# Performance work log

Measured on AMD Instinct MI355X. Metric: run time of the kernel, lower is better.

The kernel has to match this reference:

```python
import jax, jax.numpy as jnp
import numpy as np

STEP_PRI = 0.01
STEP_DUAL = 0.01
REG_SP = 0.002
NUM_ITERS = 50
B, N = 512, 64


def _matrix_power(m, p):
    # exponentiation by squaring; p is a static Python int >= 1
    result = jnp.broadcast_to(jnp.eye(m.shape[-1], dtype=m.dtype), m.shape)
    while p > 0:
        if p & 1:
            result = result @ m
        p >>= 1
        if p:
            m = m @ m
    return result


def _matrix_poly(m, d, p):
    # (I + m/d)^p, matching torch matrix_poly
    x = jnp.eye(d, dtype=m.dtype) + m / d
    return _matrix_power(x, p)


def _threshold(x):
    # nn.Threshold(0.5, 0): x if x > 0.5 else 0
    return jnp.where(x > 0.5, x, jnp.zeros_like(x))


def setup_inputs() -> dict:
    key = jax.random.key(0)
    adj = jax.random.uniform(key, (B, N, N), dtype=jnp.float32)
    return {"adj": adj}


def reference(adj):
    n = adj.shape[-1]
    x0 = adj
    scores = _threshold(adj)
    alpha0 = jnp.zeros(adj.shape[0], dtype=adj.dtype)

    def step(carry, _):
        x, alpha = carry
        # grad of augmented Lagrangian (DAG constraint gradient uses (I + x*x/n)^(n-1)^T)
        poly_t = jnp.swapaxes(_matrix_poly(x * x, n, n - 1), -1, -2)
        grad = -scores + 2.0 * alpha[:, None, None] * x * poly_t / n
        til_x = x - STEP_PRI * grad
        # soft-threshold (prox of L1), then clamp to <= 1
        new_x = jax.nn.relu(jnp.abs(til_x) - REG_SP * STEP_PRI)
        x = 1.0 - jax.nn.relu(1.0 - new_x)
        # constraint2: tr((I + x*x/n)^min(30,n)) / n - 1, per batch element
        h = jnp.trace(_matrix_poly(x * x, n, min(30, n)), axis1=-2, axis2=-1) / n - 1.0
        alpha = alpha + STEP_DUAL * h
        return (x, alpha), None

    (x, _), _ = jax.lax.scan(step, (x0, alpha0), None, length=NUM_ITERS)
    return _threshold(x)
```

## Files before the change

kernel.cpp:

```cpp
#include <hip/hip_runtime.h>
#include <stdint.h>

#define PL 4096

typedef unsigned int u32;
typedef unsigned short u16;
typedef float f32x4 __attribute__((ext_vector_type(4)));
typedef short short8 __attribute__((ext_vector_type(8)));
typedef unsigned int u32x2 __attribute__((ext_vector_type(2)));

__device__ __forceinline__ u32 prm(u32 a, u32 b, u32 s) {
  return __builtin_amdgcn_perm(a, b, s);
}
__device__ __forceinline__ u32 pk(float f0, float f1) {
  return prm(__float_as_uint(f1), __float_as_uint(f0), 0x07060302u);
}
__device__ __forceinline__ float rlo(u32 w) { return __uint_as_float(w << 16); }
__device__ __forceinline__ float rhi(u32 w) {
  return __uint_as_float(w & 0xffff0000u);
}
__device__ __forceinline__ short8 mk8(u32 w0, u32 w1, u32 w2, u32 w3) {
  union {
    u32 w[4];
    short8 s;
  } u;
  u.w[0] = w0;
  u.w[1] = w1;
  u.w[2] = w2;
  u.w[3] = w3;
  return u.s;
}
__device__ __forceinline__ void dot8(short8 a, short8 b, float& part) {
  union {
    short8 s;
    u32 w[4];
  } ua, ub;
  ua.s = a;
  ub.s = b;
#pragma unroll
  for (int w = 0; w < 4; ++w) {
    part = fmaf(rlo(ua.w[w]), rlo(ub.w[w]), part);
    part = fmaf(rhi(ua.w[w]), rhi(ub.w[w]), part);
  }
}
__device__ __forceinline__ f32x4 MF(short8 a, short8 b, f32x4 c) {
  return __builtin_amdgcn_mfma_f32_16x16x32_bf16(a, b, c, 0, 0, 0);
}

struct AF {
  short8 a0, a1;
};
struct BF8 {
  short8 b[4][2];
};

__device__ __forceinline__ void dist2(u32 U, u32 V, u32& x, u32& y) {
  u32x2 s = __builtin_amdgcn_permlane32_swap(U, V, false, false);
#if __has_builtin(__builtin_amdgcn_permlane16_swap)
  u32x2 t = __builtin_amdgcn_permlane16_swap(s[0], s[1], false, false);
  x = t[0];
  y = t[1];
#else
  u32 a = s[0], b = s[1];
  u32 bx = (u32)__shfl_xor((int)b, 16);
  u32 ax = (u32)__shfl_xor((int)a, 16);
  const bool odd = ((threadIdx.x >> 4) & 1) != 0;
  x = odd ? bx : a;
  y = odd ? b : ax;
#endif
}

__device__ __forceinline__ AF macc_to_af(const f32x4 (&m)[4]) {
  u32 P0[4], P1[4];
#pragma unroll
  for (int b = 0; b < 4; ++b) {
    P0[b] = pk(m[b][0], m[b][1]);
    P1[b] = pk(m[b][2], m[b][3]);
  }
  u32 W0[4], W1[4];
  dist2(P0[0], P0[1], W0[0], W0[2]);
  dist2(P1[0], P1[1], W0[1], W0[3]);
  dist2(P0[2], P0[3], W1[0], W1[2]);
  dist2(P1[2], P1[3], W1[1], W1[3]);
  AF r;
  r.a0 = mk8(W0[0], W0[1], W0[2], W0[3]);
  r.a1 = mk8(W1[0], W1[1], W1[2], W1[3]);
  return r;
}

__global__ __launch_bounds__(256, 2) void dag_iter_kernel(
    const float* __restrict__ adj, float* __restrict__ out) {
  __shared__ __align__(16) u16 BUF[4 * PL];
  __shared__ float red[4];
  u16* S0 = BUF;
  u16* S1 = BUF + PL;
  u16* S2 = BUF + 2 * PL;
  u16* S3 = BUF + 3 * PL;

  if ((blockIdx.x >> 8) & 1) __builtin_amdgcn_s_sleep(11);

  const int tid = (int)threadIdx.x;
  const int lane = tid & 63;
  const int wv = tid >> 6;
  const int l15 = lane & 15;
  const int grp = lane >> 4;
  const int l7 = l15 & 7;
  const int r0 = (tid & 15) << 2;
  const int c0 = (((tid >> 4) + (tid & 15)) & 15) << 2;

  int ra[2];
#pragma unroll
  for (int kh = 0; kh < 2; ++kh)
    ra[kh] = (16 * wv + l15) * 64 + ((((kh << 2) + grp) ^ l7) << 3);
  int rb[4][2];
#pragma unroll
  for (int b = 0; b < 4; ++b)
#pragma unroll
    for (int kh = 0; kh < 2; ++kh)
      rb[b][kh] = (16 * b + l15) * 64 + ((((kh << 2) + grp) ^ l7) << 3);
  int sT[4];
#pragma unroll
  for (int b = 0; b < 4; ++b)
    sT[b] = (16 * b + l15) * 64 + (((2 * wv + (grp >> 1)) ^ l7) << 3) +
            ((grp & 1) << 2);
  int prow[4], pcol[4];
#pragma unroll
  for (int i = 0; i < 4; ++i) {
    prow[i] = (r0 + i) * 64 + ((((c0 >> 3) ^ ((r0 + i) & 7))) << 3) + (c0 & 7);
    pcol[i] = (c0 + i) * 64 + ((((r0 >> 3) ^ ((c0 + i) & 7))) << 3) + (r0 & 7);
  }

  const float* src = adj + (size_t)blockIdx.x * 4096;
  float x[4][4], sc[4][4];
#pragma unroll
  for (int i = 0; i < 4; ++i) {
    f32x4 v = *(const f32x4*)(src + (r0 + i) * 64 + c0);
#pragma unroll
    for (int j = 0; j < 4; ++j) {
      x[i][j] = v[j];
      sc[i][j] = (v[j] > 0.5f) ? v[j] : 0.0f;
    }
  }
  float alpha = 0.0f;
  AF af;
  BF8 bf3;

  auto loadBF = [&](const u16* P) {
    BF8 f;
#pragma unroll
    for (int b = 0; b < 4; ++b) {
      f.b[b][0] = *(const short8*)(P + rb[b][0]);
      f.b[b][1] = *(const short8*)(P + rb[b][1]);
    }
    return f;
  };
  auto mirrorAF = [&](const AF& a, const BF8& bf) {
    const f32x4 Z = {0.0f, 0.0f, 0.0f, 0.0f};
    f32x4 m[4];
    __builtin_amdgcn_s_setprio(1);
#pragma unroll
    for (int b = 0; b < 4; ++b) {
      m[b] = MF(bf.b[b][0], a.a0, Z);
      m[b] = MF(bf.b[b][1], a.a1, m[b]);
    }
    __builtin_amdgcn_s_setprio(0);
    return macc_to_af(m);
  };
  auto primaryT = [&](const AF& a, const BF8& bf, u16* P) {
    const f32x4 Z = {0.0f, 0.0f, 0.0f, 0.0f};
    f32x4 p[4];
    __builtin_amdgcn_s_setprio(1);
#pragma unroll
    for (int b = 0; b < 4; ++b) {
      p[b] = MF(a.a0, bf.b[b][0], Z);
      p[b] = MF(a.a1, bf.b[b][1], p[b]);
    }
    __builtin_amdgcn_s_setprio(0);
#pragma unroll
    for (int b = 0; b < 4; ++b)
      *(uint2*)(P + sT[b]) = make_uint2(pk(p[b][0], p[b][1]), pk(p[b][2], p[b][3]));
  };
  auto traceP = [&](const AF& a, const BF8& bf) {
    short8 c0s = bf.b[0][0], c1s = bf.b[0][1];
    if (wv == 1) {
      c0s = bf.b[1][0];
      c1s = bf.b[1][1];
    } else if (wv == 2) {
      c0s = bf.b[2][0];
      c1s = bf.b[2][1];
    } else if (wv == 3) {
      c0s = bf.b[3][0];
      c1s = bf.b[3][1];
    }
    float part = 0.0f;
    dot8(a.a0, c0s, part);
    dot8(a.a1, c1s, part);
#pragma unroll
    for (int off = 1; off < 64; off <<= 1) part += __shfl_xor(part, off);
    if (lane == 0) red[wv] = part;
  };

  auto prox = [&](float til[4][4]) {
#pragma unroll
    for (int i = 0; i < 4; ++i)
#pragma unroll
      for (int j = 0; j < 4; ++j) {
        float ax = fabsf(til[i][j]) - 2e-5f;
        x[i][j] = fminf(fmaxf(ax, 0.0f), 1.0f);
      }
  };
  auto stage = [&]() {
    float m[4][4];
#pragma unroll
    for (int i = 0; i < 4; ++i)
#pragma unroll
      for (int j = 0; j < 4; ++j)
        m[i][j] = fmaf(x[i][j] * x[i][j], 0.015625f,
                       (r0 + i == c0 + j) ? 1.0f : 0.0f);
#pragma unroll
    for (int i = 0; i < 4; ++i)
      *(uint2*)(S0 + prow[i]) =
          make_uint2(pk(m[i][0], m[i][1]), pk(m[i][2], m[i][3]));
#pragma unroll
    for (int j = 0; j < 4; ++j)
      *(uint2*)(S1 + pcol[j]) =
          make_uint2(pk(m[0][j], m[1][j]), pk(m[2][j], m[3][j]));
    __syncthreads();
  };
  auto gradprox = [&]() {
    float tr = red[0] + red[1] + red[2] + red[3];
    alpha = fmaf(0.01f, tr * 0.015625f - 1.0f, alpha);
    const float a2 = alpha * 0.03125f;
    float til[4][4];
#pragma unroll
    for (int i = 0; i < 4; ++i) {
      uint2 w = *(const uint2*)(S2 + prow[i]);
      float pt[4] = {rlo(w.x), rhi(w.x), rlo(w.y), rhi(w.y)};
#pragma unroll
      for (int j = 0; j < 4; ++j) {
        float g = fmaf(a2 * x[i][j], pt[j], -sc[i][j]);
        til[i][j] = fmaf(-0.01f, g, x[i][j]);
      }
    }
    prox(til);
  };

  auto chain = [&]() {
    AF afm;
    afm.a0 = *(const short8*)(S0 + ra[0]);
    afm.a1 = *(const short8*)(S0 + ra[1]);
    BF8 bm = loadBF(S1);
    AF af2 = mirrorAF(afm, bm);
    AF af3 = mirrorAF(af2, bm);
    primaryT(af2, bm, S2);
    __syncthreads();
    bf3 = loadBF(S2);
    AF af6 = mirrorAF(af3, bf3);
    AF af9 = mirrorAF(af6, bf3);
    AF af12 = mirrorAF(af9, bf3);
    af = mirrorAF(af12, bf3);
    primaryT(af12, bf3, S3);
    __syncthreads();
  };
  auto front = [&]() {
    BF8 b15 = loadBF(S3);
    traceP(af, b15);
    AF af30 = mirrorAF(af, b15);
    AF af45 = mirrorAF(af30, b15);
    AF af60 = mirrorAF(af45, b15);
    primaryT(af60, bf3, S2);
    __syncthreads();
  };

  {
    float til[4][4];
#pragma unroll
    for (int i = 0; i < 4; ++i)
#pragma unroll
      for (int j = 0; j < 4; ++j) til[i][j] = fmaf(0.01f, sc[i][j], x[i][j]);
    prox(til);
    stage();
    chain();
  }
  for (int it = 0; it < 48; ++it) {
    front();
    gradprox();
    stage();
    chain();
  }
  front();
  gradprox();

  float* dst = out + (size_t)blockIdx.x * 4096;
#pragma unroll
  for (int i = 0; i < 4; ++i) {
    f32x4 v;
#pragma unroll
    for (int j = 0; j < 4; ++j) v[j] = (x[i][j] > 0.5f) ? x[i][j] : 0.0f;
    *(f32x4*)(dst + (r0 + i) * 64 + c0) = v;
  }
}

extern "C" void kernel_launch(void* const* d_in, const int* in_sizes, int n_in,
                              void* d_out, int out_size, void* d_ws,
                              size_t ws_size, hipStream_t stream) {
  const float* adj = (const float*)d_in[0];
  float* out = (float*)d_out;
  const int nbatch = in_sizes[0] / 4096;
  dag_iter_kernel<<<nbatch, 256, 0, stream>>>(adj, out);
}
```

Baseline: 213.1 us.

## Permute K-dimension storage layout to eliminate permlane shuffles in MFMA chaining

Reorders the logical-to-physical column/K mapping of the staged matrices so that MFMA accumulator outputs can be packed directly into the next MFMA's A-operand without cross-lane permlane swaps. The staging addresses, transposed stores and global load/store columns are remapped consistently to the permuted index order. This removes the permlane32/16 swap instructions on every chained matrix multiply, at the cost of a more intricate index mapping that must stay consistent everywhere.

```diff
diff --git a/kernel.cpp b/kernel.cpp
--- a/kernel.cpp
+++ b/kernel.cpp
@@ -7,7 +7,6 @@
 typedef unsigned short u16;
 typedef float f32x4 __attribute__((ext_vector_type(4)));
 typedef short short8 __attribute__((ext_vector_type(8)));
-typedef unsigned int u32x2 __attribute__((ext_vector_type(2)));
 
 __device__ __forceinline__ u32 prm(u32 a, u32 b, u32 s) {
   return __builtin_amdgcn_perm(a, b, s);
@@ -54,22 +53,6 @@
   short8 b[4][2];
 };
 
-__device__ __forceinline__ void dist2(u32 U, u32 V, u32& x, u32& y) {
-  u32x2 s = __builtin_amdgcn_permlane32_swap(U, V, false, false);
-#if __has_builtin(__builtin_amdgcn_permlane16_swap)
-  u32x2 t = __builtin_amdgcn_permlane16_swap(s[0], s[1], false, false);
-  x = t[0];
-  y = t[1];
-#else
-  u32 a = s[0], b = s[1];
-  u32 bx = (u32)__shfl_xor((int)b, 16);
-  u32 ax = (u32)__shfl_xor((int)a, 16);
-  const bool odd = ((threadIdx.x >> 4) & 1) != 0;
-  x = odd ? bx : a;
-  y = odd ? b : ax;
-#endif
-}
-
 __device__ __forceinline__ AF macc_to_af(const f32x4 (&m)[4]) {
   u32 P0[4], P1[4];
 #pragma unroll
@@ -77,14 +60,9 @@
     P0[b] = pk(m[b][0], m[b][1]);
     P1[b] = pk(m[b][2], m[b][3]);
   }
-  u32 W0[4], W1[4];
-  dist2(P0[0], P0[1], W0[0], W0[2]);
-  dist2(P1[0], P1[1], W0[1], W0[3]);
-  dist2(P0[2], P0[3], W1[0], W1[2]);
-  dist2(P1[2], P1[3], W1[1], W1[3]);
   AF r;
-  r.a0 = mk8(W0[0], W0[1], W0[2], W0[3]);
-  r.a1 = mk8(W1[0], W1[1], W1[2], W1[3]);
+  r.a0 = mk8(P0[0], P1[0], P0[1], P1[1]);
+  r.a1 = mk8(P0[2], P1[2], P0[3], P1[3]);
   return r;
 }
 
@@ -105,8 +83,15 @@
   const int l15 = lane & 15;
   const int grp = lane >> 4;
   const int l7 = l15 & 7;
-  const int r0 = (tid & 15) << 2;
-  const int c0 = (((tid >> 4) + (tid & 15)) & 15) << 2;
+
+  const int rq = tid & 15;
+  const int r0 = rq << 2;
+  const int yq = (((tid >> 4) + rq) & 15);
+  const int yb = yq << 2;
+  const int cq = ((yq >> 1) & 3) + ((yq & 1) << 2) + ((yq >> 3) << 3);
+  const int c0g = cq << 2;
+  const int rpq = ((rq & 3) << 1) + ((rq >> 2) & 1) + ((rq >> 3) << 3);
+  const int rp0 = rpq << 2;
 
   int ra[2];
 #pragma unroll
@@ -121,20 +106,22 @@
   int sT[4];
 #pragma unroll
   for (int b = 0; b < 4; ++b)
-    sT[b] = (16 * b + l15) * 64 + (((2 * wv + (grp >> 1)) ^ l7) << 3) +
-            ((grp & 1) << 2);
+    sT[b] = (16 * b + l15) * 64 +
+            ((((grp + ((wv >> 1) << 2)) ^ ((16 * b + l15) & 7))) << 3) +
+            ((wv & 1) << 2);
   int prow[4], pcol[4];
 #pragma unroll
   for (int i = 0; i < 4; ++i) {
-    prow[i] = (r0 + i) * 64 + ((((c0 >> 3) ^ ((r0 + i) & 7))) << 3) + (c0 & 7);
-    pcol[i] = (c0 + i) * 64 + ((((r0 >> 3) ^ ((c0 + i) & 7))) << 3) + (r0 & 7);
+    prow[i] = (r0 + i) * 64 + ((((yb >> 3) ^ ((r0 + i) & 7))) << 3) + (yb & 7);
+    pcol[i] =
+        (c0g + i) * 64 + ((((rp0 >> 3) ^ ((c0g + i) & 7))) << 3) + (rp0 & 7);
   }
 
   const float* src = adj + (size_t)blockIdx.x * 4096;
   float x[4][4], sc[4][4];
 #pragma unroll
   for (int i = 0; i < 4; ++i) {
-    f32x4 v = *(const f32x4*)(src + (r0 + i) * 64 + c0);
+    f32x4 v = *(const f32x4*)(src + (r0 + i) * 64 + c0g);
 #pragma unroll
     for (int j = 0; j < 4; ++j) {
       x[i][j] = v[j];
@@ -178,7 +165,8 @@
     __builtin_amdgcn_s_setprio(0);
 #pragma unroll
     for (int b = 0; b < 4; ++b)
-      *(uint2*)(P + sT[b]) = make_uint2(pk(p[b][0], p[b][1]), pk(p[b][2], p[b][3]));
+      *(uint2*)(P + sT[b]) =
+          make_uint2(pk(p[b][0], p[b][1]), pk(p[b][2], p[b][3]));
   };
   auto traceP = [&](const AF& a, const BF8& bf) {
     short8 c0s = bf.b[0][0], c1s = bf.b[0][1];
@@ -216,7 +204,7 @@
 #pragma unroll
       for (int j = 0; j < 4; ++j)
         m[i][j] = fmaf(x[i][j] * x[i][j], 0.015625f,
-                       (r0 + i == c0 + j) ? 1.0f : 0.0f);
+                       (r0 + i == c0g + j) ? 1.0f : 0.0f);
 #pragma unroll
     for (int i = 0; i < 4; ++i)
       *(uint2*)(S0 + prow[i]) =
@@ -297,7 +285,7 @@
     f32x4 v;
 #pragma unroll
     for (int j = 0; j < 4; ++j) v[j] = (x[i][j] > 0.5f) ? x[i][j] : 0.0f;
-    *(f32x4*)(dst + (r0 + i) * 64 + c0) = v;
+    *(f32x4*)(dst + (r0 + i) * 64 + c0g) = v;
   }
 }
 
```

Measured after the change: 189.9 us. 1.12x faster.
